# Performance work log

Measured on AMD Instinct MI355X. Metric: run time of the kernel, lower is better.

The kernel has to match this reference:

```python
import jax, jax.numpy as jnp
import numpy as np

# ---- static config matching init_kwargs / input_specs ----
B, H, W_IN, IN_CAPS, ATOMS = 2, 48, 48, 8, 16
KER, STRIDE, OUT_CAPS, ROUTINGS = 3, 1, 16, 3


def setup_inputs() -> dict:
    key = jax.random.key(0)
    k1, k2 = jax.random.split(key)
    x = jax.random.normal(k1, (B, H, W_IN, IN_CAPS * (ATOMS + 1)), dtype=jnp.float32)
    # W: [input_num_capsule, num_capsule, 4, 4], he_normal-ish scale (fan_in=16)
    W = jax.random.normal(k2, (IN_CAPS, OUT_CAPS, 4, 4), dtype=jnp.float32) * np.float32((2.0 / 16.0) ** 0.5)
    return {"input_tensor": x, "W": W}


def _kernel_tile(x, k=KER, stride=STRIDE):
    # Equivalent to the depthwise-conv patch-extraction trick + transpose:
    # output [B, Ho, Wo, k*k, C]
    b, h, w, c = x.shape
    ho = (h - k) // stride + 1
    wo = (w - k) // stride + 1
    patches = jnp.stack(
        [x[:, i:i + stride * ho:stride, j:j + stride * wo:stride, :]
         for i in range(k) for j in range(k)],
        axis=3,
    )
    return patches


def _squash(s, eps=1e-7):
    sq = jnp.sum(s * s, axis=-1, keepdims=True)
    return (sq / (1.0 + sq)) * s / jnp.sqrt(sq + eps)


def reference(input_tensor, W):
    t = _kernel_tile(input_tensor)                      # [B,Ho,Wo,kk,C]
    b, ho, wo, kk, c = t.shape
    n = b * ho * wo
    t = t.reshape(n, kk * IN_CAPS, ATOMS + 1)           # [N, kk*in_caps, 17]
    pose = t[..., :ATOMS].reshape(n, kk, IN_CAPS, 4, 4)
    act = t[..., ATOMS].reshape(n, kk * IN_CAPS)        # input capsule activations
    # vote transform: pose @ W per (input capsule -> output capsule)
    votes = jnp.einsum('nkiab,iobc->nkioac', pose, W)
    votes = votes.reshape(n, kk * IN_CAPS, OUT_CAPS, ATOMS)  # [N, kkin, out, 16]
    # iterative routing-by-agreement, weighted by input activation
    logits = jnp.zeros((n, kk * IN_CAPS, OUT_CAPS), dtype=votes.dtype)
    v = None
    for r in range(ROUTINGS):
        coup = jax.nn.softmax(logits, axis=2) * act[:, :, None]
        s = jnp.einsum('nko,nkoe->noe', coup, votes)    # weighted vote sum
        v = _squash(s)                                  # [N, out, 16]
        if r < ROUTINGS - 1:
            logits = logits + jnp.einsum('nkoe,noe->nko', votes, v)
    return v.reshape(b, ho, wo, OUT_CAPS, ATOMS)
```

## Files before the change

kernel.cpp:

```cpp
#include <hip/hip_runtime.h>


#define IN_CAPS 8
#define OUT_CAPS 16
#define KK 9
#define KKIN 72
#define BATCH 2
#define H_IN 48
#define W_IN 48
#define HO 46
#define WO 46
#define CIN 136
#define NPIX (BATCH*HO*WO)

typedef float v2f __attribute__((ext_vector_type(2)));
typedef float v4f __attribute__((ext_vector_type(4)));

__device__ __forceinline__ v2f lo2(v4f v) { return __builtin_shufflevector(v, v, 0, 1); }
__device__ __forceinline__ v2f hi2(v4f v) { return __builtin_shufflevector(v, v, 2, 3); }
__device__ __forceinline__ v2f fma2(v2f a, v2f b, v2f c) {
    return __builtin_elementwise_fma(a, b, c);
}

template<int CTRL>
__device__ __forceinline__ float dpp_f(float x) {
    return __int_as_float(
        __builtin_amdgcn_update_dpp(0, __float_as_int(x), CTRL, 0xF, 0xF, true));
}
__device__ __forceinline__ float row_sum16(float x) {
    x += dpp_f<0xB1>(x);
    x += dpp_f<0x4E>(x);
    x += dpp_f<0x124>(x);
    x += dpp_f<0x128>(x);
    return x;
}

__device__ __forceinline__ int g_row(int o, int ic) {
    return (o * 8 + ic) * 20 + o * 8;
}

__global__ __launch_bounds__(256, 4)
void capsule_routing_kernel(const float* __restrict__ x,
                            const float* __restrict__ Wg,
                            float* __restrict__ out)
{
    __shared__ alignas(16) float pose_t[16 * 76];
    __shared__ alignas(16) float g_s[2676];
    __shared__ alignas(16) float coup_s[OUT_CAPS * 72];
    __shared__ float act_s[KKIN];

    const int tid = threadIdx.x;
    const int o = tid >> 4;
    const int e = tid & 15;
    const int c = e & 3;

    const int n   = blockIdx.x;
    const int b   = n / (HO * WO);
    const int rem = n - b * (HO * WO);
    const int ho  = rem / WO;
    const int wo  = rem - ho * WO;

    v2f w01[IN_CAPS], w23[IN_CAPS];
    #pragma unroll
    for (int i = 0; i < IN_CAPS; ++i) {
        const v4f wv = *reinterpret_cast<const v4f*>(
            &Wg[((i * OUT_CAPS + o) * 4 + c) * 4]);
        w01[i] = lo2(wv);
        w23[i] = hi2(wv);
    }

    for (int idx = tid; idx < KK * CIN; idx += 256) {
        int p  = idx / CIN;
        int cc = idx - p * CIN;
        int py = p / 3, px = p - py * 3;
        float val = x[(((b * H_IN + ho + py) * W_IN) + (wo + px)) * CIN + cc];
        int ic = cc / 17;
        int aa = cc - ic * 17;
        int k  = p * IN_CAPS + ic;
        if (aa == 16) {
            act_s[k] = val;
            const float cv = val * 0.0625f;
            #pragma unroll
            for (int j = 0; j < OUT_CAPS; ++j) coup_s[j * 72 + k] = cv;
        } else {
            pose_t[aa * 76 + k] = val;
        }
    }
    __syncthreads();

    const int kf  = tid >> 1;
    const int hf  = tid & 1;
    const int ick = kf & 7;
    float lreg8[8] = {0.f,0.f,0.f,0.f,0.f,0.f,0.f,0.f};

    const v4f* cp = reinterpret_cast<const v4f*>(&coup_s[o * 72]);
    const v4f* pp = reinterpret_cast<const v4f*>(&pose_t[e * 76]);

    float v = 0.f;
    #pragma unroll 1
    for (int r = 0; r < 3; ++r) {
        v2f M01 = {0.f,0.f}, M23 = {0.f,0.f}, M45 = {0.f,0.f}, M67 = {0.f,0.f};
        #pragma unroll
        for (int p = 0; p < KK; ++p) {
            const v4f c0 = cp[2*p], c1 = cp[2*p+1];
            const v4f q0 = pp[2*p], q1 = pp[2*p+1];
            M01 = fma2(lo2(c0), lo2(q0), M01);
            M23 = fma2(hi2(c0), hi2(q0), M23);
            M45 = fma2(lo2(c1), lo2(q1), M45);
            M67 = fma2(hi2(c1), hi2(q1), M67);
        }
        const float Mc[8] = {M01.x, M01.y, M23.x, M23.y,
                             M45.x, M45.y, M67.x, M67.y};
        v2f U01 = {0.f,0.f}, U23 = {0.f,0.f};
        #pragma unroll
        for (int ic = 0; ic < 8; ++ic) {
            const v2f mm = {Mc[ic], Mc[ic]};
            U01 = fma2(w01[ic], mm, U01);
            U23 = fma2(w23[ic], mm, U23);
        }
        float Z0 = U01.x, Z1 = U01.y, Z2 = U23.x, Z3 = U23.y;
        Z0 += dpp_f<0xB1>(Z0); Z1 += dpp_f<0xB1>(Z1);
        Z2 += dpp_f<0xB1>(Z2); Z3 += dpp_f<0xB1>(Z3);
        Z0 += dpp_f<0x4E>(Z0); Z1 += dpp_f<0x4E>(Z1);
        Z2 += dpp_f<0x4E>(Z2); Z3 += dpp_f<0x4E>(Z3);
        const float s = (c == 0) ? Z0 : (c == 1) ? Z1 : (c == 2) ? Z2 : Z3;

        const float sq = row_sum16(s * s);
        v = s * (sq / ((1.f + sq) * sqrtf(sq + 1e-7f)));

        if (r < 2) {
            const float vq0 = dpp_f<0x00>(v);
            const float vq1 = dpp_f<0x55>(v);
            const float vq2 = dpp_f<0xAA>(v);
            const float vq3 = dpp_f<0xFF>(v);
            const v2f vq01 = {vq0, vq1};
            const v2f vq23 = {vq2, vq3};
            #pragma unroll
            for (int ic = 0; ic < 8; ++ic) {
                v2f h = fma2(w23[ic], vq23, w01[ic] * vq01);
                g_s[g_row(o, ic) + e] = h.x + h.y;
            }
            __syncthreads();
            if (tid < 2 * KKIN) {
                float q[16];
                #pragma unroll
                for (int j = 0; j < 16; ++j) q[j] = pose_t[j * 76 + kf];
                const v2f q0 = {q[0],  q[1]},  q1 = {q[2],  q[3]};
                const v2f q2 = {q[4],  q[5]},  q3 = {q[6],  q[7]};
                const v2f q4 = {q[8],  q[9]},  q5 = {q[10], q[11]};
                const v2f q6 = {q[12], q[13]}, q7 = {q[14], q[15]};
                float lg[8];
                #pragma unroll
                for (int j = 0; j < 8; ++j) {
                    const int oo = hf * 8 + j;
                    const v4f* gp = reinterpret_cast<const v4f*>(
                        &g_s[g_row(oo, ick)]);
                    const v4f g0 = gp[0], g1 = gp[1], g2 = gp[2], g3 = gp[3];
                    v2f A = fma2(q2, lo2(g1), fma2(q4, lo2(g2),
                              fma2(q6, lo2(g3), q0 * lo2(g0))));
                    v2f Bv = fma2(q3, hi2(g1), fma2(q5, hi2(g2),
                              fma2(q7, hi2(g3), q1 * hi2(g0))));
                    lreg8[j] += (A.x + A.y) + (Bv.x + Bv.y);
                    lg[j] = lreg8[j];
                }
                float mx = -1e30f;
                #pragma unroll
                for (int j = 0; j < 8; ++j) mx = fmaxf(mx, lg[j]);
                mx = fmaxf(mx, dpp_f<0xB1>(mx));
                float sum = 0.f;
                #pragma unroll
                for (int j = 0; j < 8; ++j) { lg[j] = __expf(lg[j] - mx); sum += lg[j]; }
                sum += dpp_f<0xB1>(sum);
                const float scale = act_s[kf] / sum;
                #pragma unroll
                for (int j = 0; j < 8; ++j)
                    coup_s[(hf * 8 + j) * 72 + kf] = lg[j] * scale;
            }
            __syncthreads();
        }
    }

    out[n * 256 + tid] = v;
}

extern "C" void kernel_launch(void* const* d_in, const int* in_sizes, int n_in,
                              void* d_out, int out_size, void* d_ws, size_t ws_size,
                              hipStream_t stream) {
    const float* x  = (const float*)d_in[0];
    const float* Wt = (const float*)d_in[1];
    float* outp = (float*)d_out;
    capsule_routing_kernel<<<dim3(NPIX), dim3(256), 0, stream>>>(x, Wt, outp);
}
```

Baseline: 98.91 us.

## Process one pixel per wavefront to remove block-wide barriers

Restructures the kernel so each 64-lane wavefront handles one output pixel, with four pixels per 256-thread block and per-wave shared memory slices. Each lane now computes four output atoms, so __syncthreads is replaced by lgkmcnt waits and cross-lane swizzle reductions. Block indices are also remapped across XCDs, and the initial uniform coupling is folded into a scale factor. It aims to cut barrier and idle-thread overhead, in exchange for more registers per lane and lower launch-bounds occupancy.

```diff
diff --git a/kernel.cpp b/kernel.cpp
--- a/kernel.cpp
+++ b/kernel.cpp
@@ -1,17 +1,8 @@
 #include <hip/hip_runtime.h>
 
 
-#define IN_CAPS 8
-#define OUT_CAPS 16
-#define KK 9
-#define KKIN 72
-#define BATCH 2
-#define H_IN 48
-#define W_IN 48
-#define HO 46
-#define WO 46
-#define CIN 136
-#define NPIX (BATCH*HO*WO)
+#define NPIX 4232
+#define NBLK 1058
 
 typedef float v2f __attribute__((ext_vector_type(2)));
 typedef float v4f __attribute__((ext_vector_type(4)));
@@ -27,160 +18,237 @@
     return __int_as_float(
         __builtin_amdgcn_update_dpp(0, __float_as_int(x), CTRL, 0xF, 0xF, true));
 }
-__device__ __forceinline__ float row_sum16(float x) {
-    x += dpp_f<0xB1>(x);
-    x += dpp_f<0x4E>(x);
-    x += dpp_f<0x124>(x);
-    x += dpp_f<0x128>(x);
-    return x;
+template<int OFF>
+__device__ __forceinline__ float swz(float x) {
+    return __int_as_float(__builtin_amdgcn_ds_swizzle(__float_as_int(x), OFF));
 }
 
 __device__ __forceinline__ int g_row(int o, int ic) {
-    return (o * 8 + ic) * 20 + o * 8;
-}
-
-__global__ __launch_bounds__(256, 4)
+    return (o * 8 + ic) * 20 + o * 4;
+}
+
+__global__ __launch_bounds__(256, 2)
 void capsule_routing_kernel(const float* __restrict__ x,
                             const float* __restrict__ Wg,
                             float* __restrict__ out)
 {
-    __shared__ alignas(16) float pose_t[16 * 76];
-    __shared__ alignas(16) float g_s[2676];
-    __shared__ alignas(16) float coup_s[OUT_CAPS * 72];
-    __shared__ float act_s[KKIN];
-
-    const int tid = threadIdx.x;
-    const int o = tid >> 4;
-    const int e = tid & 15;
-    const int c = e & 3;
-
-    const int n   = blockIdx.x;
-    const int b   = n / (HO * WO);
-    const int rem = n - b * (HO * WO);
-    const int ho  = rem / WO;
-    const int wo  = rem - ho * WO;
-
-    v2f w01[IN_CAPS], w23[IN_CAPS];
-    #pragma unroll
-    for (int i = 0; i < IN_CAPS; ++i) {
+    __shared__ alignas(16) float pose_t[4][1288];
+    __shared__ alignas(16) float coup_s[4][1216];
+    __shared__ alignas(16) float g_s[4][2616];
+
+    const int tid  = threadIdx.x;
+    const int wid  = tid >> 6;
+    const int lane = tid & 63;
+    const int o    = lane >> 2;
+    const int cq   = lane & 3;
+
+    float* PT = pose_t[wid];
+    float* CP = coup_s[wid];
+    float* G  = g_s[wid];
+
+    const int bx  = blockIdx.x;
+    const int xcd = bx & 7;
+    const int sub = bx >> 3;
+    const int wgs = (xcd < 2 ? xcd * 133 : 266 + (xcd - 2) * 132) + sub;
+    const int n   = wgs * 4 + wid;
+
+    const int b   = n / (46 * 46);
+    const int rem = n - b * (46 * 46);
+    const int ho  = rem / 46;
+    const int wo  = rem - ho * 46;
+
+    v2f w01[8], w23[8];
+    #pragma unroll
+    for (int i = 0; i < 8; ++i) {
         const v4f wv = *reinterpret_cast<const v4f*>(
-            &Wg[((i * OUT_CAPS + o) * 4 + c) * 4]);
+            &Wg[((i * 16 + o) * 4 + cq) * 4]);
         w01[i] = lo2(wv);
         w23[i] = hi2(wv);
     }
 
-    for (int idx = tid; idx < KK * CIN; idx += 256) {
-        int p  = idx / CIN;
-        int cc = idx - p * CIN;
-        int py = p / 3, px = p - py * 3;
-        float val = x[(((b * H_IN + ho + py) * W_IN) + (wo + px)) * CIN + cc];
-        int ic = cc / 17;
-        int aa = cc - ic * 17;
-        int k  = p * IN_CAPS + ic;
-        if (aa == 16) {
-            act_s[k] = val;
-            const float cv = val * 0.0625f;
-            #pragma unroll
-            for (int j = 0; j < OUT_CAPS; ++j) coup_s[j * 72 + k] = cv;
-        } else {
-            pose_t[aa * 76 + k] = val;
-        }
-    }
-    __syncthreads();
-
-    const int kf  = tid >> 1;
-    const int hf  = tid & 1;
-    const int ick = kf & 7;
-    float lreg8[8] = {0.f,0.f,0.f,0.f,0.f,0.f,0.f,0.f};
-
-    const v4f* cp = reinterpret_cast<const v4f*>(&coup_s[o * 72]);
-    const v4f* pp = reinterpret_cast<const v4f*>(&pose_t[e * 76]);
-
-    float v = 0.f;
+    #pragma unroll
+    for (int p = 0; p < 9; ++p) {
+        const int py = p / 3, px = p - py * 3;
+        const float* xr = &x[(((b * 48) + ho + py) * 48 + (wo + px)) * 136];
+        #pragma unroll
+        for (int t = 0; t < 3; ++t) {
+            const int cc = lane + t * 64;
+            if (t < 2 || cc < 136) {
+                const float val = xr[cc];
+                const int ic = (cc * 241) >> 12;
+                const int aa = cc - ic * 17;
+                const int k  = p * 8 + ic;
+                if (aa == 16) PT[1216 + k] = val;
+                else          PT[aa * 76 + k] = val;
+            }
+        }
+    }
+    asm volatile("s_waitcnt lgkmcnt(0)" ::: "memory");
+
+    float lreg[16];
+    #pragma unroll
+    for (int j = 0; j < 16; ++j) lreg[j] = 0.f;
+    float lt0 = 0.f, lt1 = 0.f;
+
+    const int kT  = 64 + (lane >> 3);
+    const int icT = lane >> 3;
+    const int oT0 = (lane & 7) * 2;
+
+    v2f va01[4], va23[4];
+
     #pragma unroll 1
     for (int r = 0; r < 3; ++r) {
-        v2f M01 = {0.f,0.f}, M23 = {0.f,0.f}, M45 = {0.f,0.f}, M67 = {0.f,0.f};
-        #pragma unroll
-        for (int p = 0; p < KK; ++p) {
-            const v4f c0 = cp[2*p], c1 = cp[2*p+1];
-            const v4f q0 = pp[2*p], q1 = pp[2*p+1];
-            M01 = fma2(lo2(c0), lo2(q0), M01);
-            M23 = fma2(hi2(c0), hi2(q0), M23);
-            M45 = fma2(lo2(c1), lo2(q1), M45);
-            M67 = fma2(hi2(c1), hi2(q1), M67);
-        }
-        const float Mc[8] = {M01.x, M01.y, M23.x, M23.y,
-                             M45.x, M45.y, M67.x, M67.y};
-        v2f U01 = {0.f,0.f}, U23 = {0.f,0.f};
-        #pragma unroll
-        for (int ic = 0; ic < 8; ++ic) {
-            const v2f mm = {Mc[ic], Mc[ic]};
-            U01 = fma2(w01[ic], mm, U01);
-            U23 = fma2(w23[ic], mm, U23);
-        }
-        float Z0 = U01.x, Z1 = U01.y, Z2 = U23.x, Z3 = U23.y;
-        Z0 += dpp_f<0xB1>(Z0); Z1 += dpp_f<0xB1>(Z1);
-        Z2 += dpp_f<0xB1>(Z2); Z3 += dpp_f<0xB1>(Z3);
-        Z0 += dpp_f<0x4E>(Z0); Z1 += dpp_f<0x4E>(Z1);
-        Z2 += dpp_f<0x4E>(Z2); Z3 += dpp_f<0x4E>(Z3);
-        const float s = (c == 0) ? Z0 : (c == 1) ? Z1 : (c == 2) ? Z2 : Z3;
-
-        const float sq = row_sum16(s * s);
-        v = s * (sq / ((1.f + sq) * sqrtf(sq + 1e-7f)));
+        const float* cb  = (r == 0) ? (PT + 1216) : (CP + o * 76);
+        const float  msc = (r == 0) ? 0.0625f : 1.0f;
+        v2f mac[4][4];
+        #pragma unroll
+        for (int m = 0; m < 4; ++m)
+            #pragma unroll
+            for (int a = 0; a < 4; ++a) mac[m][a] = v2f{0.f, 0.f};
+        #pragma unroll
+        for (int p = 0; p < 9; ++p) {
+            const v4f c0 = *reinterpret_cast<const v4f*>(cb + 8 * p);
+            const v4f c1 = *reinterpret_cast<const v4f*>(cb + 8 * p + 4);
+            #pragma unroll
+            for (int a = 0; a < 4; ++a) {
+                const v4f q0 = *reinterpret_cast<const v4f*>(
+                    &PT[(a * 4 + cq) * 76 + 8 * p]);
+                const v4f q1 = *reinterpret_cast<const v4f*>(
+                    &PT[(a * 4 + cq) * 76 + 8 * p + 4]);
+                mac[0][a] = fma2(lo2(c0), lo2(q0), mac[0][a]);
+                mac[1][a] = fma2(hi2(c0), hi2(q0), mac[1][a]);
+                mac[2][a] = fma2(lo2(c1), lo2(q1), mac[2][a]);
+                mac[3][a] = fma2(hi2(c1), hi2(q1), mac[3][a]);
+            }
+        }
+        v2f U01[4], U23[4];
+        #pragma unroll
+        for (int a = 0; a < 4; ++a) { U01[a] = v2f{0.f,0.f}; U23[a] = v2f{0.f,0.f}; }
+        #pragma unroll
+        for (int m = 0; m < 4; ++m) {
+            #pragma unroll
+            for (int a = 0; a < 4; ++a) {
+                const v2f m0 = { mac[m][a].x, mac[m][a].x };
+                const v2f m1 = { mac[m][a].y, mac[m][a].y };
+                U01[a] = fma2(w01[2*m],   m0, U01[a]);
+                U23[a] = fma2(w23[2*m],   m0, U23[a]);
+                U01[a] = fma2(w01[2*m+1], m1, U01[a]);
+                U23[a] = fma2(w23[2*m+1], m1, U23[a]);
+            }
+        }
+        float Z[16];
+        #pragma unroll
+        for (int a = 0; a < 4; ++a) {
+            Z[a*4+0] = U01[a].x * msc;  Z[a*4+1] = U01[a].y * msc;
+            Z[a*4+2] = U23[a].x * msc;  Z[a*4+3] = U23[a].y * msc;
+        }
+        #pragma unroll
+        for (int j = 0; j < 16; ++j) {
+            Z[j] += dpp_f<0xB1>(Z[j]);
+            Z[j] += dpp_f<0x4E>(Z[j]);
+        }
+        float sq = 0.f;
+        #pragma unroll
+        for (int j = 0; j < 16; ++j) sq = fmaf(Z[j], Z[j], sq);
+        const float ss = sq / ((1.f + sq) * sqrtf(sq + 1e-7f));
+        #pragma unroll
+        for (int a = 0; a < 4; ++a) {
+            va01[a] = v2f{ Z[a*4+0] * ss, Z[a*4+1] * ss };
+            va23[a] = v2f{ Z[a*4+2] * ss, Z[a*4+3] * ss };
+        }
 
         if (r < 2) {
-            const float vq0 = dpp_f<0x00>(v);
-            const float vq1 = dpp_f<0x55>(v);
-            const float vq2 = dpp_f<0xAA>(v);
-            const float vq3 = dpp_f<0xFF>(v);
-            const v2f vq01 = {vq0, vq1};
-            const v2f vq23 = {vq2, vq3};
             #pragma unroll
             for (int ic = 0; ic < 8; ++ic) {
-                v2f h = fma2(w23[ic], vq23, w01[ic] * vq01);
-                g_s[g_row(o, ic) + e] = h.x + h.y;
-            }
-            __syncthreads();
-            if (tid < 2 * KKIN) {
-                float q[16];
                 #pragma unroll
-                for (int j = 0; j < 16; ++j) q[j] = pose_t[j * 76 + kf];
-                const v2f q0 = {q[0],  q[1]},  q1 = {q[2],  q[3]};
-                const v2f q2 = {q[4],  q[5]},  q3 = {q[6],  q[7]};
-                const v2f q4 = {q[8],  q[9]},  q5 = {q[10], q[11]};
-                const v2f q6 = {q[12], q[13]}, q7 = {q[14], q[15]};
-                float lg[8];
-                #pragma unroll
-                for (int j = 0; j < 8; ++j) {
-                    const int oo = hf * 8 + j;
-                    const v4f* gp = reinterpret_cast<const v4f*>(
-                        &g_s[g_row(oo, ick)]);
+                for (int a = 0; a < 4; ++a) {
+                    const v2f h = fma2(w23[ic], va23[a], w01[ic] * va01[a]);
+                    G[g_row(o, ic) + a * 4 + cq] = h.x + h.y;
+                }
+            }
+            float pc[16], pcT[16];
+            #pragma unroll
+            for (int j = 0; j < 16; ++j) pc[j]  = PT[j * 76 + lane];
+            #pragma unroll
+            for (int j = 0; j < 16; ++j) pcT[j] = PT[j * 76 + kT];
+            const float actk = PT[1216 + lane];
+            const float actT = PT[1216 + kT];
+            asm volatile("s_waitcnt lgkmcnt(0)" ::: "memory");
+
+            const int icM = lane & 7;
+            const v2f q0 = {pc[0],  pc[1]},  q1 = {pc[2],  pc[3]};
+            const v2f q2 = {pc[4],  pc[5]},  q3 = {pc[6],  pc[7]};
+            const v2f q4 = {pc[8],  pc[9]},  q5 = {pc[10], pc[11]};
+            const v2f q6 = {pc[12], pc[13]}, q7 = {pc[14], pc[15]};
+            float lg[16];
+            #pragma unroll
+            for (int oo = 0; oo < 16; ++oo) {
+                const v4f* gp = reinterpret_cast<const v4f*>(&G[g_row(oo, icM)]);
+                const v4f g0 = gp[0], g1 = gp[1], g2 = gp[2], g3 = gp[3];
+                const v2f A  = fma2(q2, lo2(g1), fma2(q4, lo2(g2),
+                               fma2(q6, lo2(g3), q0 * lo2(g0))));
+                const v2f Bv = fma2(q3, hi2(g1), fma2(q5, hi2(g2),
+                               fma2(q7, hi2(g3), q1 * hi2(g0))));
+                lreg[oo] += (A.x + A.y) + (Bv.x + Bv.y);
+                lg[oo] = lreg[oo];
+            }
+            float mx = lg[0];
+            #pragma unroll
+            for (int j = 1; j < 16; ++j) mx = fmaxf(mx, lg[j]);
+            float sum = 0.f;
+            #pragma unroll
+            for (int j = 0; j < 16; ++j) { lg[j] = __expf(lg[j] - mx); sum += lg[j]; }
+            const float cs = actk / sum;
+            #pragma unroll
+            for (int oo = 0; oo < 16; ++oo) CP[oo * 76 + lane] = lg[oo] * cs;
+
+            {
+                const v2f t0 = {pcT[0],  pcT[1]},  t1 = {pcT[2],  pcT[3]};
+                const v2f t2 = {pcT[4],  pcT[5]},  t3 = {pcT[6],  pcT[7]};
+                const v2f t4 = {pcT[8],  pcT[9]},  t5 = {pcT[10], pcT[11]};
+                const v2f t6 = {pcT[12], pcT[13]}, t7 = {pcT[14], pcT[15]};
+                {
+                    const v4f* gp = reinterpret_cast<const v4f*>(&G[g_row(oT0, icT)]);
                     const v4f g0 = gp[0], g1 = gp[1], g2 = gp[2], g3 = gp[3];
-                    v2f A = fma2(q2, lo2(g1), fma2(q4, lo2(g2),
-                              fma2(q6, lo2(g3), q0 * lo2(g0))));
-                    v2f Bv = fma2(q3, hi2(g1), fma2(q5, hi2(g2),
-                              fma2(q7, hi2(g3), q1 * hi2(g0))));
-                    lreg8[j] += (A.x + A.y) + (Bv.x + Bv.y);
-                    lg[j] = lreg8[j];
+                    const v2f A  = fma2(t2, lo2(g1), fma2(t4, lo2(g2),
+                                   fma2(t6, lo2(g3), t0 * lo2(g0))));
+                    const v2f Bv = fma2(t3, hi2(g1), fma2(t5, hi2(g2),
+                                   fma2(t7, hi2(g3), t1 * hi2(g0))));
+                    lt0 += (A.x + A.y) + (Bv.x + Bv.y);
                 }
-                float mx = -1e30f;
-                #pragma unroll
-                for (int j = 0; j < 8; ++j) mx = fmaxf(mx, lg[j]);
-                mx = fmaxf(mx, dpp_f<0xB1>(mx));
-                float sum = 0.f;
-                #pragma unroll
-                for (int j = 0; j < 8; ++j) { lg[j] = __expf(lg[j] - mx); sum += lg[j]; }
-                sum += dpp_f<0xB1>(sum);
-                const float scale = act_s[kf] / sum;
-                #pragma unroll
-                for (int j = 0; j < 8; ++j)
-                    coup_s[(hf * 8 + j) * 72 + kf] = lg[j] * scale;
-            }
-            __syncthreads();
-        }
-    }
-
-    out[n * 256 + tid] = v;
+                {
+                    const v4f* gp = reinterpret_cast<const v4f*>(&G[g_row(oT0 + 1, icT)]);
+                    const v4f g0 = gp[0], g1 = gp[1], g2 = gp[2], g3 = gp[3];
+                    const v2f A  = fma2(t2, lo2(g1), fma2(t4, lo2(g2),
+                                   fma2(t6, lo2(g3), t0 * lo2(g0))));
+                    const v2f Bv = fma2(t3, hi2(g1), fma2(t5, hi2(g2),
+                                   fma2(t7, hi2(g3), t1 * hi2(g0))));
+                    lt1 += (A.x + A.y) + (Bv.x + Bv.y);
+                }
+                float m2 = fmaxf(lt0, lt1);
+                m2 = fmaxf(m2, swz<0x041F>(m2));
+                m2 = fmaxf(m2, swz<0x081F>(m2));
+                m2 = fmaxf(m2, swz<0x101F>(m2));
+                const float e0 = __expf(lt0 - m2);
+                const float e1 = __expf(lt1 - m2);
+                float s2 = e0 + e1;
+                s2 += swz<0x041F>(s2);
+                s2 += swz<0x081F>(s2);
+                s2 += swz<0x101F>(s2);
+                const float csT = actT / s2;
+                CP[oT0 * 76 + kT]       = e0 * csT;
+                CP[(oT0 + 1) * 76 + kT] = e1 * csT;
+            }
+            asm volatile("s_waitcnt lgkmcnt(0)" ::: "memory");
+        }
+    }
+
+    #pragma unroll
+    for (int a = 0; a < 4; ++a) {
+        const float vo = (cq & 2) ? ((cq & 1) ? va23[a].y : va23[a].x)
+                                  : ((cq & 1) ? va01[a].y : va01[a].x);
+        out[n * 256 + o * 16 + a * 4 + cq] = vo;
+    }
 }
 
 extern "C" void kernel_launch(void* const* d_in, const int* in_sizes, int n_in,
@@ -189,5 +257,5 @@
     const float* x  = (const float*)d_in[0];
     const float* Wt = (const float*)d_in[1];
     float* outp = (float*)d_out;
-    capsule_routing_kernel<<<dim3(NPIX), dim3(256), 0, stream>>>(x, Wt, outp);
-}
+    capsule_routing_kernel<<<dim3(NBLK), dim3(256), 0, stream>>>(x, Wt, outp);
+}
```

After: 95.18 us. -3.8%, faster.
